# Optimization experiments

Hardware: AMD Instinct MI355X
Metric: run time of the kernel (lower is better)

Reference implementation:

```python
import jax, jax.numpy as jnp
import numpy as np

N_NODES = 100000
N_EDGES = 1600000
D_FEAT = 64
NUM_LAYERS = 3


def setup_inputs() -> dict:
    key = jax.random.key(0)
    k1, k2, k3, k4 = jax.random.split(key, 4)
    X = jax.random.normal(k1, (N_NODES, D_FEAT), dtype=jnp.float32)
    src = jax.random.randint(k2, (N_EDGES,), 0, N_NODES, dtype=jnp.int32)
    dst = jax.random.randint(k3, (N_EDGES,), 0, N_NODES, dtype=jnp.int32)
    ew = jax.random.uniform(k4, (N_EDGES,), dtype=jnp.float32)
    return {"X": X, "src": src, "dst": dst, "ew": ew}


def _spmm(X, src, dst, ew):
    # gather source features, scale by edge weight, scatter-sum into dst
    msgs = X[src] * ew[:, None]  # [E, d]
    return jax.ops.segment_sum(msgs, dst, num_segments=N_NODES)


def reference(X, src, dst, ew):
    # LightGCNConv with stack_layers=True: average of layer-0..num_layers embeddings
    X_list = [X]
    h = X
    for _ in range(NUM_LAYERS):
        h = _spmm(h, src, dst, ew)
        X_list.append(h)
    return jnp.mean(jnp.stack(X_list, axis=1), axis=1)  # [N, d]
```

## Files before the change

kernel.cpp:

```cpp
#include <hip/hip_runtime.h>
#include <hip/hip_fp16.h>

#define N_NODES 100000
#define D_FEAT  64
#define N_EDGES 1600000
#define NPB     128
#define NBUCK   ((N_NODES + NPB - 1) / NPB)
#define CAP     3072
#define CVT_BLOCKS  500
#define CVT_THREADS 1024
#define CHUNK   (N_EDGES / CVT_BLOCKS)
#define PULL_BLOCKS 2048
#define WCAP    64

__global__ void init_bcur(int* __restrict__ bcur) {
    int t = threadIdx.x;
    if (t < NBUCK) bcur[t] = 0;
}

__global__ __launch_bounds__(CVT_THREADS) void cvt_part(const float* __restrict__ X,
                                                        __half* __restrict__ Xh,
                                                        const int* __restrict__ src,
                                                        const int* __restrict__ dst,
                                                        const float* __restrict__ ew,
                                                        int* __restrict__ bcur,
                                                        int2* __restrict__ edges_p) {
    __shared__ int h[NBUCK];
    const int t = threadIdx.x;
    for (int i = t; i < NBUCK; i += CVT_THREADS) h[i] = 0;

    const int n4 = N_NODES * D_FEAT / 4;
    for (int i = blockIdx.x * CVT_THREADS + t; i < n4; i += CVT_BLOCKS * CVT_THREADS) {
        float4 v = ((const float4*)X)[i];
        ((__half2*)Xh)[2 * i]     = __floats2half2_rn(v.x, v.y);
        ((__half2*)Xh)[2 * i + 1] = __floats2half2_rn(v.z, v.w);
    }
    __syncthreads();

    const int beg = blockIdx.x * CHUNK;
    const int base = beg + 4 * t;
    const bool act = (4 * t < CHUNK);

    int4 d4;
    if (act) {
        d4 = *(const int4*)(dst + base);
        atomicAdd(&h[d4.x >> 7], 1);
        atomicAdd(&h[d4.y >> 7], 1);
        atomicAdd(&h[d4.z >> 7], 1);
        atomicAdd(&h[d4.w >> 7], 1);
    }
    __syncthreads();

    if (t < NBUCK) {
        int c = h[t];
        h[t] = c ? atomicAdd(&bcur[t], c) : 0;
    }
    __syncthreads();

    if (act) {
        int4   s4 = *(const int4*)(src + base);
        float4 w4 = *(const float4*)(ew + base);
        int b, p;
        b = d4.x >> 7; p = atomicAdd(&h[b], 1);
        if (p < CAP) edges_p[(size_t)b * CAP + p] = make_int2(s4.x | ((d4.x & 127) << 17), __float_as_int(w4.x));
        b = d4.y >> 7; p = atomicAdd(&h[b], 1);
        if (p < CAP) edges_p[(size_t)b * CAP + p] = make_int2(s4.y | ((d4.y & 127) << 17), __float_as_int(w4.y));
        b = d4.z >> 7; p = atomicAdd(&h[b], 1);
        if (p < CAP) edges_p[(size_t)b * CAP + p] = make_int2(s4.z | ((d4.z & 127) << 17), __float_as_int(w4.z));
        b = d4.w >> 7; p = atomicAdd(&h[b], 1);
        if (p < CAP) edges_p[(size_t)b * CAP + p] = make_int2(s4.w | ((d4.w & 127) << 17), __float_as_int(w4.w));
    }
}

__global__ __launch_bounds__(256) void sort_bucket(int2* __restrict__ edges_p,
                                                   const int* __restrict__ bcur,
                                                   int2* __restrict__ nodeptr) {
    __shared__ int cnt[NPB], sc[NPB], cur[NPB];
    __shared__ int2 buf[CAP];
    const int b = blockIdx.x, t = threadIdx.x;
    const int beg = b * CAP;
    int n = bcur[b];
    if (n > CAP) n = CAP;

    if (t < NPB) cnt[t] = 0;
    __syncthreads();
    for (int i = t; i < n; i += 256) {
        int2 e = edges_p[beg + i];
        buf[i] = e;
        atomicAdd(&cnt[e.x >> 17], 1);
    }
    __syncthreads();

    if (t < NPB) sc[t] = cnt[t];
    __syncthreads();
    for (int off = 1; off < NPB; off <<= 1) {
        int v = (t >= off && t < NPB) ? sc[t - off] : 0;
        __syncthreads();
        if (t < NPB) sc[t] += v;
        __syncthreads();
    }
    if (t < NPB) {
        cur[t] = sc[t] - cnt[t];
        int node = b * NPB + t;
        if (node < N_NODES) nodeptr[node] = make_int2(beg + sc[t] - cnt[t], cnt[t]);
    }
    __syncthreads();

    for (int i = t; i < n; i += 256) {
        int2 e = buf[i];
        int p = atomicAdd(&cur[e.x >> 17], 1);
        edges_p[beg + p] = make_int2(e.x & 0x1FFFF, e.y);
    }
}

template <int MODE>
__global__ __launch_bounds__(256) void spmm_pull(const __half* __restrict__ hprev,
                                                 const int2* __restrict__ nodeptr,
                                                 const int2* __restrict__ edges,
                                                 __half* __restrict__ hout,
                                                 float* __restrict__ out,
                                                 const float* __restrict__ X,
                                                 const __half* __restrict__ h1,
                                                 const __half* __restrict__ h2) {
    __shared__ int2 ebuf[4][WCAP];
    const int t    = threadIdx.x;
    const int wid  = t >> 6;
    const int lane = t & 63;
    const int half = lane >> 5;
    const int sub  = lane & 31;
    const int gw     = blockIdx.x * 4 + wid;
    const int nwaves = gridDim.x * 4;

    for (int node = gw; node < N_NODES; node += nwaves) {
        int2 np = nodeptr[node];
        const int beg = np.x, d = np.y;

        if (d <= WCAP) {
            const int dp = (d + 15) & ~15;
            if (lane < dp) {
                int2 e = (lane < d) ? edges[beg + lane] : make_int2(0, 0);
                ebuf[wid][lane] = e;
            }
            float ax = 0.0f, ay = 0.0f;
            const int nb = dp >> 4;
            for (int bi = 0; bi < nb; ++bi) {
                const int base = bi * 16 + half;
                unsigned tv[8]; float w[8];
                #pragma unroll
                for (int k = 0; k < 8; ++k) {
                    int2 e = ebuf[wid][base + 2 * k];
                    w[k]  = __int_as_float(e.y);
                    tv[k] = *(const unsigned*)(hprev + (((size_t)e.x << 6) | (2 * sub)));
                }
                #pragma unroll
                for (int k = 0; k < 8; ++k) {
                    float2 f = __half22float2(*(__half2*)&tv[k]);
                    ax += f.x * w[k];
                    ay += f.y * w[k];
                }
            }
            ax += __shfl_xor(ax, 32);
            ay += __shfl_xor(ay, 32);
            if (half == 0) {
                size_t bo = (size_t)node * 32 + sub;
                if (MODE == 2) {
                    float2 x  = ((const float2*)X)[bo];
                    float2 f1 = __half22float2(((const __half2*)h1)[bo]);
                    float2 f2 = __half22float2(((const __half2*)h2)[bo]);
                    ((float2*)out)[bo] = make_float2((x.x + f1.x + f2.x + ax) * 0.25f,
                                                     (x.y + f1.y + f2.y + ay) * 0.25f);
                } else {
                    ((__half2*)hout)[bo] = __floats2half2_rn(ax, ay);
                }
            }
        } else {
            const int end = beg + d;
            float ax = 0.0f, ay = 0.0f;
            for (int j = beg; j < end; j += 16) {
                unsigned tv[8]; float w[8];
                #pragma unroll
                for (int k = 0; k < 8; ++k) {
                    int i0 = j + 2 * k, i1 = i0 + 1;
                    int2 e0 = edges[(i0 < end) ? i0 : beg];
                    int2 e1 = edges[(i1 < end) ? i1 : beg];
                    int s = half ? e1.x : e0.x;
                    float w0 = (i0 < end) ? __int_as_float(e0.y) : 0.0f;
                    float w1 = (i1 < end) ? __int_as_float(e1.y) : 0.0f;
                    w[k] = half ? w1 : w0;
                    tv[k] = *(const unsigned*)(hprev + (((size_t)s << 6) | (2 * sub)));
                }
                #pragma unroll
                for (int k = 0; k < 8; ++k) {
                    float2 f = __half22float2(*(__half2*)&tv[k]);
                    ax += f.x * w[k];
                    ay += f.y * w[k];
                }
            }
            ax += __shfl_xor(ax, 32);
            ay += __shfl_xor(ay, 32);
            if (half == 0) {
                size_t bo = (size_t)node * 32 + sub;
                if (MODE == 2) {
                    float2 x  = ((const float2*)X)[bo];
                    float2 f1 = __half22float2(((const __half2*)h1)[bo]);
                    float2 f2 = __half22float2(((const __half2*)h2)[bo]);
                    ((float2*)out)[bo] = make_float2((x.x + f1.x + f2.x + ax) * 0.25f,
                                                     (x.y + f1.y + f2.y + ay) * 0.25f);
                } else {
                    ((__half2*)hout)[bo] = __floats2half2_rn(ax, ay);
                }
            }
        }
    }
}

extern "C" void kernel_launch(void* const* d_in, const int* in_sizes, int n_in,
                              void* d_out, int out_size, void* d_ws, size_t ws_size,
                              hipStream_t stream) {
    const float* X   = (const float*)d_in[0];
    const int*   src = (const int*)  d_in[1];
    const int*   dst = (const int*)  d_in[2];
    const float* ew  = (const float*)d_in[3];
    float* out = (float*)d_out;

    const size_t feat = (size_t)N_NODES * D_FEAT;

    char* p = (char*)d_ws;
    __half* hA      = (__half*)p; p += feat * sizeof(__half);
    __half* hB      = (__half*)p; p += feat * sizeof(__half);
    __half* Xh      = (__half*)p; p += feat * sizeof(__half);
    int2*  edges_p  = (int2*)p;   p += (size_t)NBUCK * CAP * sizeof(int2);
    int2*  nodeptr  = (int2*)p;   p += (size_t)N_NODES * sizeof(int2);
    int*   bcur     = (int*)p;    p += (size_t)NBUCK * 4;

    init_bcur  <<<1, 1024, 0, stream>>>(bcur);
    cvt_part   <<<CVT_BLOCKS, CVT_THREADS, 0, stream>>>(X, Xh, src, dst, ew, bcur, edges_p);
    sort_bucket<<<NBUCK, 256, 0, stream>>>(edges_p, bcur, nodeptr);

    spmm_pull<0><<<PULL_BLOCKS, 256, 0, stream>>>(Xh, nodeptr, edges_p, hA, out, X, hA, hB);
    spmm_pull<1><<<PULL_BLOCKS, 256, 0, stream>>>(hA, nodeptr, edges_p, hB, out, X, hA, hB);
    spmm_pull<2><<<PULL_BLOCKS, 256, 0, stream>>>(hB, nodeptr, edges_p, (__half*)nullptr, out, X, hA, hB);
}
```

Measured before the change: 222.9 us.

## Pack edges into 32-bit words with 15-bit quantized weights and prefetch node pointers

Sorted edges are now stored as one 32-bit word holding a 17-bit source index and a 15-bit fixed-point weight, which halves edge traffic in the three pull passes. The pull loop also prefetches the node pointers and edge words of the next nodes in software, and reads the shared edge buffer with paired loads. Weight quantization adds error on top of the existing fp16 features, and any weight at or above 1.0 would be clamped.

```diff
diff --git a/kernel.cpp b/kernel.cpp
--- a/kernel.cpp
+++ b/kernel.cpp
@@ -72,8 +72,9 @@
     }
 }
 
-__global__ __launch_bounds__(256) void sort_bucket(int2* __restrict__ edges_p,
+__global__ __launch_bounds__(256) void sort_bucket(const int2* __restrict__ edges_p,
                                                    const int* __restrict__ bcur,
+                                                   unsigned* __restrict__ sedges,
                                                    int2* __restrict__ nodeptr) {
     __shared__ int cnt[NPB], sc[NPB], cur[NPB];
     __shared__ int2 buf[CAP];
@@ -109,48 +110,66 @@
     for (int i = t; i < n; i += 256) {
         int2 e = buf[i];
         int p = atomicAdd(&cur[e.x >> 17], 1);
-        edges_p[beg + p] = make_int2(e.x & 0x1FFFF, e.y);
+        float wf = __int_as_float(e.y);
+        unsigned wq = (unsigned)(wf * 32768.0f + 0.5f);
+        if (wq > 32767u) wq = 32767u;
+        sedges[beg + p] = (unsigned)(e.x & 0x1FFFF) | (wq << 17);
     }
 }
 
 template <int MODE>
 __global__ __launch_bounds__(256) void spmm_pull(const __half* __restrict__ hprev,
                                                  const int2* __restrict__ nodeptr,
-                                                 const int2* __restrict__ edges,
+                                                 const unsigned* __restrict__ edges,
                                                  __half* __restrict__ hout,
                                                  float* __restrict__ out,
                                                  const float* __restrict__ X,
                                                  const __half* __restrict__ h1,
                                                  const __half* __restrict__ h2) {
-    __shared__ int2 ebuf[4][WCAP];
+    __shared__ unsigned ebuf[4][WCAP];
     const int t    = threadIdx.x;
     const int wid  = t >> 6;
     const int lane = t & 63;
     const int half = lane >> 5;
     const int sub  = lane & 31;
     const int gw     = blockIdx.x * 4 + wid;
-    const int nwaves = gridDim.x * 4;
-
-    for (int node = gw; node < N_NODES; node += nwaves) {
-        int2 np = nodeptr[node];
-        const int beg = np.x, d = np.y;
+    const int stride = gridDim.x * 4;
+    const float S = 1.0f / 32768.0f;
+
+    int node = gw;
+    if (node >= N_NODES) return;
+
+    int2 np_c = nodeptr[node];
+    int n1 = node + stride;
+    int2 np_n = (n1 < N_NODES) ? nodeptr[n1] : make_int2(0, 0);
+    unsigned er_c = (np_c.y <= WCAP && lane < np_c.y) ? edges[np_c.x + lane] : 0u;
+
+    for (; node < N_NODES; node += stride) {
+        const int beg = np_c.x, d = np_c.y;
+
+        int nn2 = node + 2 * stride;
+        int2 np_nn = (nn2 < N_NODES) ? nodeptr[nn2] : make_int2(0, 0);
+        unsigned er_n = (np_n.y <= WCAP && lane < np_n.y) ? edges[np_n.x + lane] : 0u;
 
         if (d <= WCAP) {
             const int dp = (d + 15) & ~15;
-            if (lane < dp) {
-                int2 e = (lane < d) ? edges[beg + lane] : make_int2(0, 0);
-                ebuf[wid][lane] = e;
-            }
+            if (lane < dp) ebuf[wid][lane] = er_c;
             float ax = 0.0f, ay = 0.0f;
             const int nb = dp >> 4;
             for (int bi = 0; bi < nb; ++bi) {
-                const int base = bi * 16 + half;
+                const int base = bi * 16 + half * 8;
+                unsigned e[8];
+                #pragma unroll
+                for (int k = 0; k < 4; ++k) {
+                    uint2 p2 = *(const uint2*)&ebuf[wid][base + 2 * k];
+                    e[2 * k]     = p2.x;
+                    e[2 * k + 1] = p2.y;
+                }
                 unsigned tv[8]; float w[8];
                 #pragma unroll
                 for (int k = 0; k < 8; ++k) {
-                    int2 e = ebuf[wid][base + 2 * k];
-                    w[k]  = __int_as_float(e.y);
-                    tv[k] = *(const unsigned*)(hprev + (((size_t)e.x << 6) | (2 * sub)));
+                    w[k]  = (float)(e[k] >> 17);
+                    tv[k] = *(const unsigned*)(hprev + (((size_t)(e[k] & 0x1FFFF) << 6) | (2 * sub)));
                 }
                 #pragma unroll
                 for (int k = 0; k < 8; ++k) {
@@ -163,54 +182,51 @@
             ay += __shfl_xor(ay, 32);
             if (half == 0) {
                 size_t bo = (size_t)node * 32 + sub;
+                float fx = ax * S, fy = ay * S;
                 if (MODE == 2) {
                     float2 x  = ((const float2*)X)[bo];
                     float2 f1 = __half22float2(((const __half2*)h1)[bo]);
                     float2 f2 = __half22float2(((const __half2*)h2)[bo]);
-                    ((float2*)out)[bo] = make_float2((x.x + f1.x + f2.x + ax) * 0.25f,
-                                                     (x.y + f1.y + f2.y + ay) * 0.25f);
+                    ((float2*)out)[bo] = make_float2((x.x + f1.x + f2.x + fx) * 0.25f,
+                                                     (x.y + f1.y + f2.y + fy) * 0.25f);
                 } else {
-                    ((__half2*)hout)[bo] = __floats2half2_rn(ax, ay);
+                    ((__half2*)hout)[bo] = __floats2half2_rn(fx, fy);
                 }
             }
         } else {
             const int end = beg + d;
             float ax = 0.0f, ay = 0.0f;
             for (int j = beg; j < end; j += 16) {
-                unsigned tv[8]; float w[8];
                 #pragma unroll
                 for (int k = 0; k < 8; ++k) {
-                    int i0 = j + 2 * k, i1 = i0 + 1;
-                    int2 e0 = edges[(i0 < end) ? i0 : beg];
-                    int2 e1 = edges[(i1 < end) ? i1 : beg];
-                    int s = half ? e1.x : e0.x;
-                    float w0 = (i0 < end) ? __int_as_float(e0.y) : 0.0f;
-                    float w1 = (i1 < end) ? __int_as_float(e1.y) : 0.0f;
-                    w[k] = half ? w1 : w0;
-                    tv[k] = *(const unsigned*)(hprev + (((size_t)s << 6) | (2 * sub)));
-                }
-                #pragma unroll
-                for (int k = 0; k < 8; ++k) {
-                    float2 f = __half22float2(*(__half2*)&tv[k]);
-                    ax += f.x * w[k];
-                    ay += f.y * w[k];
+                    int idx = j + half * 8 + k;
+                    unsigned ee = (idx < end) ? edges[idx] : 0u;
+                    float wk = (float)(ee >> 17);
+                    unsigned tvk = *(const unsigned*)(hprev + (((size_t)(ee & 0x1FFFF) << 6) | (2 * sub)));
+                    float2 f = __half22float2(*(__half2*)&tvk);
+                    ax += f.x * wk;
+                    ay += f.y * wk;
                 }
             }
             ax += __shfl_xor(ax, 32);
             ay += __shfl_xor(ay, 32);
             if (half == 0) {
                 size_t bo = (size_t)node * 32 + sub;
+                float fx = ax * S, fy = ay * S;
                 if (MODE == 2) {
                     float2 x  = ((const float2*)X)[bo];
                     float2 f1 = __half22float2(((const __half2*)h1)[bo]);
                     float2 f2 = __half22float2(((const __half2*)h2)[bo]);
-                    ((float2*)out)[bo] = make_float2((x.x + f1.x + f2.x + ax) * 0.25f,
-                                                     (x.y + f1.y + f2.y + ay) * 0.25f);
+                    ((float2*)out)[bo] = make_float2((x.x + f1.x + f2.x + fx) * 0.25f,
+                                                     (x.y + f1.y + f2.y + fy) * 0.25f);
                 } else {
-                    ((__half2*)hout)[bo] = __floats2half2_rn(ax, ay);
+                    ((__half2*)hout)[bo] = __floats2half2_rn(fx, fy);
                 }
             }
         }
+        np_c = np_n;
+        np_n = np_nn;
+        er_c = er_n;
     }
 }
 
@@ -230,14 +246,15 @@
     __half* hB      = (__half*)p; p += feat * sizeof(__half);
     __half* Xh      = (__half*)p; p += feat * sizeof(__half);
     int2*  edges_p  = (int2*)p;   p += (size_t)NBUCK * CAP * sizeof(int2);
+    unsigned* sedges= (unsigned*)p; p += (size_t)NBUCK * CAP * sizeof(unsigned);
     int2*  nodeptr  = (int2*)p;   p += (size_t)N_NODES * sizeof(int2);
     int*   bcur     = (int*)p;    p += (size_t)NBUCK * 4;
 
     init_bcur  <<<1, 1024, 0, stream>>>(bcur);
     cvt_part   <<<CVT_BLOCKS, CVT_THREADS, 0, stream>>>(X, Xh, src, dst, ew, bcur, edges_p);
-    sort_bucket<<<NBUCK, 256, 0, stream>>>(edges_p, bcur, nodeptr);
-
-    spmm_pull<0><<<PULL_BLOCKS, 256, 0, stream>>>(Xh, nodeptr, edges_p, hA, out, X, hA, hB);
-    spmm_pull<1><<<PULL_BLOCKS, 256, 0, stream>>>(hA, nodeptr, edges_p, hB, out, X, hA, hB);
-    spmm_pull<2><<<PULL_BLOCKS, 256, 0, stream>>>(hB, nodeptr, edges_p, (__half*)nullptr, out, X, hA, hB);
-}
+    sort_bucket<<<NBUCK, 256, 0, stream>>>(edges_p, bcur, sedges, nodeptr);
+
+    spmm_pull<0><<<PULL_BLOCKS, 256, 0, stream>>>(Xh, nodeptr, sedges, hA, out, X, hA, hB);
+    spmm_pull<1><<<PULL_BLOCKS, 256, 0, stream>>>(hA, nodeptr, sedges, hB, out, X, hA, hB);
+    spmm_pull<2><<<PULL_BLOCKS, 256, 0, stream>>>(hB, nodeptr, sedges, (__half*)nullptr, out, X, hA, hB);
+}
```

Result: no change. 227.0 us (+1.8%).
